# Kernel tuning notes

Hardware: AMD Instinct MI355X
Metric: run time of the kernel (lower is better)

Reference implementation:

```python
import jax, jax.numpy as jnp
import numpy as np

N = 50000      # nodes
E = 800000     # edges
F_IN = 128     # num_node_features
H = 128        # dim_h
C = 5          # num_classes
G = 8          # graphs in batch


def setup_inputs() -> dict:
    key = jax.random.key(0)
    ks = jax.random.split(key, 9)
    x = jax.random.normal(ks[0], (N, F_IN), dtype=jnp.float32)
    edge_index = jax.random.randint(ks[1], (2, E), 0, N, dtype=jnp.int64)
    batch = jnp.sort(jax.random.randint(ks[2], (N,), 0, G, dtype=jnp.int64))
    s1 = 1.0 / np.sqrt(F_IN)
    s2 = 1.0 / np.sqrt(H)
    sl = 1.0 / np.sqrt(2 * H)
    W1 = jax.random.uniform(ks[3], (F_IN, H), jnp.float32, -s1, s1)
    b1 = jnp.zeros((H,), jnp.float32)
    W2 = jax.random.uniform(ks[4], (H, H), jnp.float32, -s2, s2)
    b2 = jnp.zeros((H,), jnp.float32)
    Wl = jax.random.uniform(ks[5], (2 * H, C), jnp.float32, -sl, sl)
    bl = jax.random.uniform(ks[6], (C,), jnp.float32, -sl, sl)
    return {"x": x, "edge_index": edge_index, "batch": batch,
            "W1": W1, "b1": b1, "W2": W2, "b2": b2, "Wl": Wl, "bl": bl}


def gcn_conv(x, W, b, src, dst):
    # PyG GCNConv: X' = D^{-1/2} (A + I) D^{-1/2} X W + b
    xw = x @ W                                           # [N, H]
    # degree with self-loops: 1 + in-degree
    deg = jnp.ones((N,), xw.dtype).at[dst].add(1.0)      # [N]
    dinv = jax.lax.rsqrt(deg)                            # [N]
    norm = dinv[src] * dinv[dst]                         # [E]
    msg = xw[src] * norm[:, None]                        # [E, H] gather
    agg = jax.ops.segment_sum(msg, dst, num_segments=N)  # scatter-add
    agg = agg + xw * (dinv * dinv)[:, None]              # self-loop term
    return agg + b


def reference(x, edge_index, batch, W1, b1, W2, b2, Wl, bl):
    src, dst = edge_index[0], edge_index[1]
    # dropout p=0.6 is a no-op in eval mode
    h1 = jax.nn.relu(gcn_conv(x, W1, b1, src, dst))
    h2 = jax.nn.relu(gcn_conv(h1, W2, b2, src, dst))
    h = jnp.concatenate([h2, h1], axis=-1)               # [N, 2H]
    cnt = jax.ops.segment_sum(jnp.ones((N,), h.dtype), batch, num_segments=G)
    hG = jax.ops.segment_sum(h, batch, num_segments=G) / jnp.maximum(cnt, 1.0)[:, None]
    logits = hG @ Wl + bl                                # [G, C]
    return hG, jax.nn.log_softmax(logits, axis=1)
```

## Files before the change

### kernel.cpp

```cpp
#include <hip/hip_runtime.h>

#define N_NODES 50000
#define N_EDGES 800000
#define HDIM    128
#define NGRAPH  8
#define NCLS    5
#define SCAN_CHUNK 1024
#define NSCANBLK ((N_NODES + SCAN_CHUNK - 1) / SCAN_CHUNK)
#define NB_GEMM  ((N_NODES + 63) / 64)
#define NB_EDGE  ((N_EDGES + 255) / 256)

__device__ __forceinline__ float bf2f(ushort u) {
    return __uint_as_float((unsigned int)u << 16);
}
__device__ __forceinline__ ushort f2bf(float f) {
    unsigned int u = __float_as_uint(f);
    u += 0x7FFFu + ((u >> 16) & 1u);
    return (ushort)(u >> 16);
}

typedef __attribute__((ext_vector_type(8)))  __bf16 bf16x8;
typedef __attribute__((ext_vector_type(16))) float  f32x16;
typedef __attribute__((ext_vector_type(2)))  float  f32x2;
union BF8 { uint4 q; ushort u[8]; bf16x8 v; };

__global__ __launch_bounds__(256) void k_pre(const float* __restrict__ x,
                                             ushort* __restrict__ xb,
                                             const float* __restrict__ W1,
                                             const float* __restrict__ W2,
                                             ushort* __restrict__ Wt1,
                                             ushort* __restrict__ Wt2,
                                             int* cnti, float* hG) {
    int i = blockIdx.x * blockDim.x + threadIdx.x;
    if (i < N_NODES) cnti[i] = 0;
    if (i < NGRAPH * 2 * HDIM) hG[i] = 0.0f;
    if (i < HDIM * HDIM) {
        int k = i >> 7, c = i & (HDIM - 1);
        Wt1[c * HDIM + k] = f2bf(W1[i]);
        Wt2[c * HDIM + k] = f2bf(W2[i]);
    }
    if ((size_t)i * 8 < (size_t)N_NODES * HDIM) {
        float4 f0 = reinterpret_cast<const float4*>(x)[i * 2];
        float4 f1 = reinterpret_cast<const float4*>(x)[i * 2 + 1];
        uint4 o;
        o.x = (unsigned)f2bf(f0.x) | ((unsigned)f2bf(f0.y) << 16);
        o.y = (unsigned)f2bf(f0.z) | ((unsigned)f2bf(f0.w) << 16);
        o.z = (unsigned)f2bf(f1.x) | ((unsigned)f2bf(f1.y) << 16);
        o.w = (unsigned)f2bf(f1.z) | ((unsigned)f2bf(f1.w) << 16);
        reinterpret_cast<uint4*>(xb)[i] = o;
    }
}

__global__ __launch_bounds__(256) void k_count(const int* __restrict__ dst,
                                               int* cnti,
                                               ushort* __restrict__ slot16) {
    int e4 = blockIdx.x * blockDim.x + threadIdx.x;
    if (e4 < N_EDGES / 4) {
        int4 d = reinterpret_cast<const int4*>(dst)[e4];
        ushort4 s;
        s.x = (ushort)atomicAdd(&cnti[d.x], 1);
        s.y = (ushort)atomicAdd(&cnti[d.y], 1);
        s.z = (ushort)atomicAdd(&cnti[d.z], 1);
        s.w = (ushort)atomicAdd(&cnti[d.w], 1);
        reinterpret_cast<ushort4*>(slot16)[e4] = s;
    }
}

__global__ __launch_bounds__(256) void k_scan1(const int* __restrict__ cnti,
                                               int* __restrict__ rowptr,
                                               int* __restrict__ bsum,
                                               float* __restrict__ dinv) {
    __shared__ int wsum[4];
    int tid = threadIdx.x, lane = tid & 63, wid = tid >> 6;
    int i0 = blockIdx.x * SCAN_CHUNK + tid * 4;
    int v[4];
    int tsum = 0;
#pragma unroll
    for (int p = 0; p < 4; ++p) {
        int i = i0 + p;
        v[p] = (i < N_NODES) ? cnti[i] : 0;
        if (i < N_NODES) dinv[i] = rsqrtf(1.0f + (float)v[p]);
        tsum += v[p];
    }
    int sc = tsum;
#pragma unroll
    for (int off = 1; off < 64; off <<= 1) {
        int t = __shfl_up(sc, off, 64);
        if (lane >= off) sc += t;
    }
    if (lane == 63) wsum[wid] = sc;
    __syncthreads();
    int woff = 0;
    for (int w = 0; w < wid; ++w) woff += wsum[w];
    int excl = woff + sc - tsum;
#pragma unroll
    for (int p = 0; p < 4; ++p) {
        int i = i0 + p;
        if (i < N_NODES) rowptr[i] = excl;
        excl += v[p];
    }
    if (tid == 255) bsum[blockIdx.x] = woff + sc;
}

__global__ __launch_bounds__(256) void k_scan3(int* __restrict__ rowptr,
                                               const int* __restrict__ bsum) {
    __shared__ int soff;
    int tid = threadIdx.x;
    int chunk = blockIdx.x >> 2;
    if (tid < 64) {
        int v = (tid < chunk) ? bsum[tid] : 0;
#pragma unroll
        for (int off = 32; off; off >>= 1) v += __shfl_xor(v, off, 64);
        if (tid == 0) soff = v;
    }
    __syncthreads();
    int i = blockIdx.x * 256 + tid;
    if (i < N_NODES) rowptr[i] += soff;
    if (blockIdx.x == 0 && tid == 0) rowptr[N_NODES] = N_EDGES;
}

__global__ __launch_bounds__(256) void k_gemm_fill(const ushort* __restrict__ Xb,
                                                   const ushort* __restrict__ Wt,
                                                   unsigned char* __restrict__ Y,
                                                   const int* __restrict__ src,
                                                   const int* __restrict__ dst,
                                                   const int* __restrict__ rowptr,
                                                   const ushort* __restrict__ slot16,
                                                   ushort* __restrict__ csrc16) {
    if (blockIdx.x >= NB_GEMM) {
        int e = (blockIdx.x - NB_GEMM) * 256 + threadIdx.x;
        if (e < N_EDGES) {
            int d = dst[e];
            int pos = rowptr[d] + (int)slot16[e];
            csrc16[pos] = (ushort)src[e];
        }
        return;
    }
    int tid  = threadIdx.x;
    int lane = tid & 63;
    int wv   = tid >> 6;
    int c0   = wv * 32;
    int lrow = lane & 31;
    int kgrp = lane >> 5;

    bf16x8 bfrag[8];
    {
        const ushort* wp = Wt + (size_t)(c0 + lrow) * HDIM + kgrp * 8;
#pragma unroll
        for (int kc = 0; kc < 8; ++kc) {
            BF8 t;
            t.q = *reinterpret_cast<const uint4*>(wp + kc * 16);
            bfrag[kc] = t.v;
        }
    }
#pragma unroll
    for (int chunk = 0; chunk < 2; ++chunk) {
        int m0 = blockIdx.x * 64 + chunk * 32;
        if (m0 >= N_NODES) return;
        int arow = m0 + lrow;
        if (arow > N_NODES - 1) arow = N_NODES - 1;
        const ushort* xp = Xb + (size_t)arow * HDIM + kgrp * 8;
        f32x16 acc;
#pragma unroll
        for (int i = 0; i < 16; ++i) acc[i] = 0.f;
#pragma unroll
        for (int kc = 0; kc < 8; ++kc) {
            BF8 a;
            a.q = *reinterpret_cast<const uint4*>(xp + kc * 16);
            acc = __builtin_amdgcn_mfma_f32_32x32x16_bf16(a.v, bfrag[kc], acc, 0, 0, 0);
        }
#pragma unroll
        for (int r = 0; r < 16; r += 2) {
            unsigned pk = (unsigned)__builtin_amdgcn_cvt_pk_fp8_f32(acc[r], acc[r + 1], 0, false);
            int row0 = m0 + (r & 3) + 8 * (r >> 2) + 4 * kgrp;
            if (row0 < N_NODES)
                Y[(size_t)row0 * HDIM + c0 + lrow] = (unsigned char)(pk & 0xFF);
            if (row0 + 1 < N_NODES)
                Y[(size_t)(row0 + 1) * HDIM + c0 + lrow] = (unsigned char)((pk >> 8) & 0xFF);
        }
    }
}

__global__ __launch_bounds__(256) void k_gemm(const ushort* __restrict__ Xb,
                                              const ushort* __restrict__ Wt,
                                              unsigned char* __restrict__ Y) {
    int tid  = threadIdx.x;
    int lane = tid & 63;
    int wv   = tid >> 6;
    int c0   = wv * 32;
    int lrow = lane & 31;
    int kgrp = lane >> 5;

    bf16x8 bfrag[8];
    {
        const ushort* wp = Wt + (size_t)(c0 + lrow) * HDIM + kgrp * 8;
#pragma unroll
        for (int kc = 0; kc < 8; ++kc) {
            BF8 t;
            t.q = *reinterpret_cast<const uint4*>(wp + kc * 16);
            bfrag[kc] = t.v;
        }
    }
#pragma unroll
    for (int chunk = 0; chunk < 2; ++chunk) {
        int m0 = blockIdx.x * 64 + chunk * 32;
        if (m0 >= N_NODES) return;
        int arow = m0 + lrow;
        if (arow > N_NODES - 1) arow = N_NODES - 1;
        const ushort* xp = Xb + (size_t)arow * HDIM + kgrp * 8;
        f32x16 acc;
#pragma unroll
        for (int i = 0; i < 16; ++i) acc[i] = 0.f;
#pragma unroll
        for (int kc = 0; kc < 8; ++kc) {
            BF8 a;
            a.q = *reinterpret_cast<const uint4*>(xp + kc * 16);
            acc = __builtin_amdgcn_mfma_f32_32x32x16_bf16(a.v, bfrag[kc], acc, 0, 0, 0);
        }
#pragma unroll
        for (int r = 0; r < 16; r += 2) {
            unsigned pk = (unsigned)__builtin_amdgcn_cvt_pk_fp8_f32(acc[r], acc[r + 1], 0, false);
            int row0 = m0 + (r & 3) + 8 * (r >> 2) + 4 * kgrp;
            if (row0 < N_NODES)
                Y[(size_t)row0 * HDIM + c0 + lrow] = (unsigned char)(pk & 0xFF);
            if (row0 + 1 < N_NODES)
                Y[(size_t)(row0 + 1) * HDIM + c0 + lrow] = (unsigned char)((pk >> 8) & 0xFF);
        }
    }
}

__global__ __launch_bounds__(256) void k_agg(const unsigned char* __restrict__ y,
                                             const int* __restrict__ rowptr,
                                             const ushort* __restrict__ csrc16,
                                             const float* __restrict__ dinv,
                                             const float* __restrict__ bias,
                                             ushort* __restrict__ h) {
    int node = blockIdx.x * 4 + (threadIdx.x >> 6);
    if (node >= N_NODES) return;
    int lane = threadIdx.x & 63;
    int grp  = lane >> 5;
    int fl   = lane & 31;
    int e0 = rowptr[node], e1 = rowptr[node + 1];
    float di = dinv[node];
    float a0 = 0.f, a1 = 0.f, a2 = 0.f, a3 = 0.f;
    int j = e0;
    for (; j + 8 <= e1; j += 8) {
#pragma unroll
        for (int u = 0; u < 4; ++u) {
            int s = (int)csrc16[j + u * 2 + grp];
            float w = dinv[s];
            unsigned pk = *reinterpret_cast<const unsigned*>(y + (size_t)s * HDIM + fl * 4);
            f32x2 lo = __builtin_amdgcn_cvt_pk_f32_fp8(pk, false);
            f32x2 hi = __builtin_amdgcn_cvt_pk_f32_fp8(pk, true);
            a0 = fmaf(w, lo[0], a0);
            a1 = fmaf(w, lo[1], a1);
            a2 = fmaf(w, hi[0], a2);
            a3 = fmaf(w, hi[1], a3);
        }
    }
    for (; j < e1; j += 2) {
        int jj = j + grp;
        bool valid = jj < e1;
        int s = valid ? (int)csrc16[jj] : 0;
        float w = valid ? dinv[s] : 0.f;
        unsigned pk = *reinterpret_cast<const unsigned*>(y + (size_t)s * HDIM + fl * 4);
        f32x2 lo = __builtin_amdgcn_cvt_pk_f32_fp8(pk, false);
        f32x2 hi = __builtin_amdgcn_cvt_pk_f32_fp8(pk, true);
        a0 = fmaf(w, lo[0], a0);
        a1 = fmaf(w, lo[1], a1);
        a2 = fmaf(w, hi[0], a2);
        a3 = fmaf(w, hi[1], a3);
    }
    a0 += __shfl_xor(a0, 32, 64);
    a1 += __shfl_xor(a1, 32, 64);
    a2 += __shfl_xor(a2, 32, 64);
    a3 += __shfl_xor(a3, 32, 64);
    {
        unsigned pk = *reinterpret_cast<const unsigned*>(y + (size_t)node * HDIM + fl * 4);
        f32x2 lo = __builtin_amdgcn_cvt_pk_f32_fp8(pk, false);
        f32x2 hi = __builtin_amdgcn_cvt_pk_f32_fp8(pk, true);
        a0 = fmaf(di, lo[0], a0);
        a1 = fmaf(di, lo[1], a1);
        a2 = fmaf(di, hi[0], a2);
        a3 = fmaf(di, hi[1], a3);
    }
    float r0 = fmaxf(fmaf(a0, di, bias[fl * 4 + 0]), 0.f);
    float r1 = fmaxf(fmaf(a1, di, bias[fl * 4 + 1]), 0.f);
    float r2 = fmaxf(fmaf(a2, di, bias[fl * 4 + 2]), 0.f);
    float r3 = fmaxf(fmaf(a3, di, bias[fl * 4 + 3]), 0.f);
    if (grp == 0) {
        uint2 pk;
        pk.x = (unsigned)f2bf(r0) | ((unsigned)f2bf(r1) << 16);
        pk.y = (unsigned)f2bf(r2) | ((unsigned)f2bf(r3) << 16);
        *reinterpret_cast<uint2*>(h + (size_t)node * HDIM + fl * 4) = pk;
    }
}

__global__ __launch_bounds__(256) void k_pool(const ushort* __restrict__ h2,
                                              const ushort* __restrict__ h1,
                                              const int* __restrict__ batch,
                                              float* __restrict__ hG) {
    int f  = threadIdx.x;
    const ushort* srcp = (f < HDIM) ? h2 : h1;
    int ff = f & (HDIM - 1);
    int n0 = blockIdx.x * 64;
    int n1 = min(n0 + 64, N_NODES);
    int g = batch[n0];
    float run = 0.f;
    for (int n = n0; n < n1; ++n) {
        int gn = batch[n];
        if (gn != g) {
            atomicAdd(&hG[g * 256 + f], run);
            run = 0.f;
            g = gn;
        }
        run += bf2f(srcp[(size_t)n * HDIM + ff]);
    }
    atomicAdd(&hG[g * 256 + f], run);
}

__global__ __launch_bounds__(256) void k_final(const float* __restrict__ hG,
                                               const int* __restrict__ batch,
                                               const float* __restrict__ Wl,
                                               const float* __restrict__ bl,
                                               float* __restrict__ outp) {
    __shared__ float sH[NGRAPH * 2 * HDIM];
    __shared__ float sL[NGRAPH * NCLS];
    __shared__ int   sStart[NGRAPH + 1];
    int tid = threadIdx.x;
    if (tid <= NGRAPH) {
        int lo = 0, hi = N_NODES;
        while (lo < hi) {
            int mid = (lo + hi) >> 1;
            if (batch[mid] < tid) lo = mid + 1; else hi = mid;
        }
        sStart[tid] = lo;
    }
    __syncthreads();
    for (int i = tid; i < NGRAPH * 2 * HDIM; i += 256) {
        int g = i >> 8;
        float cnt = (float)(sStart[g + 1] - sStart[g]);
        float m = hG[i] / fmaxf(cnt, 1.0f);
        sH[i] = m;
        outp[i] = m;
    }
    __syncthreads();
    if (tid < NGRAPH * NCLS) {
        int g = tid / NCLS, c = tid % NCLS;
        float acc = bl[c];
        for (int k = 0; k < 2 * HDIM; ++k)
            acc += sH[g * 256 + k] * Wl[k * NCLS + c];
        sL[tid] = acc;
    }
    __syncthreads();
    if (tid < NGRAPH) {
        float mx = -1e30f;
        for (int c = 0; c < NCLS; ++c) mx = fmaxf(mx, sL[tid * NCLS + c]);
        float se = 0.f;
        for (int c = 0; c < NCLS; ++c) se += expf(sL[tid * NCLS + c] - mx);
        float lse = logf(se) + mx;
        for (int c = 0; c < NCLS; ++c)
            outp[NGRAPH * 2 * HDIM + tid * NCLS + c] = sL[tid * NCLS + c] - lse;
    }
}

extern "C" void kernel_launch(void* const* d_in, const int* in_sizes, int n_in,
                              void* d_out, int out_size, void* d_ws, size_t ws_size,
                              hipStream_t stream) {
    const float* x    = (const float*)d_in[0];
    const int*   eidx = (const int*)d_in[1];
    const int*   batch= (const int*)d_in[2];
    const float* W1   = (const float*)d_in[3];
    const float* b1   = (const float*)d_in[4];
    const float* W2   = (const float*)d_in[5];
    const float* b2   = (const float*)d_in[6];
    const float* Wl   = (const float*)d_in[7];
    const float* bl   = (const float*)d_in[8];
    float* outp = (float*)d_out;

    const int* src = eidx;
    const int* dst = eidx + N_EDGES;

    char* ws = (char*)d_ws;
    size_t off = 0;
    auto alloc = [&](size_t bytes) -> char* {
        char* p = ws + off;
        off += (bytes + 255) & ~(size_t)255;
        return p;
    };
    ushort*        xb    = (ushort*)alloc((size_t)N_NODES * HDIM * 2);
    unsigned char* y     = (unsigned char*)alloc((size_t)N_NODES * HDIM);
    ushort*        h1    = (ushort*)alloc((size_t)N_NODES * HDIM * 2);
    ushort*        h2    = (ushort*)alloc((size_t)N_NODES * HDIM * 2);
    ushort*        Wt1   = (ushort*)alloc((size_t)HDIM * HDIM * 2);
    ushort*        Wt2   = (ushort*)alloc((size_t)HDIM * HDIM * 2);
    float*         dinv  = (float*) alloc((size_t)N_NODES * 4);
    int*           cnti  = (int*)   alloc((size_t)N_NODES * 4);
    int*           rowptr= (int*)   alloc((size_t)(N_NODES + 1) * 4);
    int*           bsum  = (int*)   alloc((size_t)NSCANBLK * 4);
    ushort*        slot16= (ushort*)alloc((size_t)N_EDGES * 2);
    ushort*        csrc16= (ushort*)alloc((size_t)N_EDGES * 2);
    float*         hG    = (float*) alloc((size_t)NGRAPH * 2 * HDIM * 4);

    k_pre  <<<(N_NODES * HDIM / 8 + 255) / 256, 256, 0, stream>>>(x, xb, W1, W2, Wt1, Wt2, cnti, hG);
    k_count<<<(N_EDGES / 4 + 255) / 256, 256, 0, stream>>>(dst, cnti, slot16);
    k_scan1<<<NSCANBLK, 256, 0, stream>>>(cnti, rowptr, bsum, dinv);
    k_scan3<<<(N_NODES + 255) / 256, 256, 0, stream>>>(rowptr, bsum);

    k_gemm_fill<<<NB_GEMM + NB_EDGE, 256, 0, stream>>>(xb, Wt1, y,
                                                       src, dst, rowptr, slot16, csrc16);
    k_agg <<<(N_NODES + 3) / 4, 256, 0, stream>>>(y, rowptr, csrc16, dinv, b1, h1);
    k_gemm<<<NB_GEMM, 256, 0, stream>>>(h1, Wt2, y);
    k_agg <<<(N_NODES + 3) / 4, 256, 0, stream>>>(y, rowptr, csrc16, dinv, b2, h2);

    k_pool <<<(N_NODES + 63) / 64, 256, 0, stream>>>(h2, h1, batch, hG);
    k_final<<<1, 256, 0, stream>>>(hG, batch, Wl, bl, outp);

    (void)in_sizes; (void)n_in; (void)out_size; (void)ws_size;
}
```

Baseline: 187.1 us.

## Pad CSR rows to multiples of eight and prescale GEMM output by dinv

Each CSR row is padded to a multiple of 8 entries, with the padding pointing at a zero row appended to y. This lets the aggregation kernel load 8 source indices per uint4 and issue 8 independent gathers with no tail branches. The GEMM epilogues now multiply rows by dinv before the fp8 conversion, which removes the per-edge dinv[s] gather and its FMA weight in aggregation. The costs are extra padded gathers of the zero row, more csrc16 storage, and a serial padding loop in the scan kernel. Prescaling before fp8 quantization also slightly changes rounding.

Result: faster. 172.7 us (-7.7%).

```diff
diff --git a/kernel.cpp b/kernel.cpp
--- a/kernel.cpp
+++ b/kernel.cpp
@@ -5,6 +5,7 @@
 #define HDIM    128
 #define NGRAPH  8
 #define NCLS    5
+#define ZROW    50000
 #define SCAN_CHUNK 1024
 #define NSCANBLK ((N_NODES + SCAN_CHUNK - 1) / SCAN_CHUNK)
 #define NB_GEMM  ((N_NODES + 63) / 64)
@@ -30,10 +31,12 @@
                                              const float* __restrict__ W2,
                                              ushort* __restrict__ Wt1,
                                              ushort* __restrict__ Wt2,
-                                             int* cnti, float* hG) {
+                                             int* cnti, float* hG,
+                                             unsigned char* __restrict__ y) {
     int i = blockIdx.x * blockDim.x + threadIdx.x;
     if (i < N_NODES) cnti[i] = 0;
     if (i < NGRAPH * 2 * HDIM) hG[i] = 0.0f;
+    if (i < 32) reinterpret_cast<unsigned*>(y + (size_t)ZROW * HDIM)[i] = 0u;
     if (i < HDIM * HDIM) {
         int k = i >> 7, c = i & (HDIM - 1);
         Wt1[c * HDIM + k] = f2bf(W1[i]);
@@ -78,8 +81,9 @@
 #pragma unroll
     for (int p = 0; p < 4; ++p) {
         int i = i0 + p;
-        v[p] = (i < N_NODES) ? cnti[i] : 0;
-        if (i < N_NODES) dinv[i] = rsqrtf(1.0f + (float)v[p]);
+        int c = (i < N_NODES) ? cnti[i] : 0;
+        if (i < N_NODES) dinv[i] = rsqrtf(1.0f + (float)c);
+        v[p] = (c + 7) & ~7;
         tsum += v[p];
     }
     int sc = tsum;
@@ -103,7 +107,9 @@
 }
 
 __global__ __launch_bounds__(256) void k_scan3(int* __restrict__ rowptr,
-                                               const int* __restrict__ bsum) {
+                                               const int* __restrict__ bsum,
+                                               const int* __restrict__ cnti,
+                                               ushort* __restrict__ csrc16) {
     __shared__ int soff;
     int tid = threadIdx.x;
     int chunk = blockIdx.x >> 2;
@@ -115,12 +121,19 @@
     }
     __syncthreads();
     int i = blockIdx.x * 256 + tid;
-    if (i < N_NODES) rowptr[i] += soff;
-    if (blockIdx.x == 0 && tid == 0) rowptr[N_NODES] = N_EDGES;
+    if (i < N_NODES) {
+        int rp = rowptr[i] + soff;
+        rowptr[i] = rp;
+        int c  = cnti[i];
+        int ce = (c + 7) & ~7;
+        for (int p = c; p < ce; ++p) csrc16[rp + p] = (ushort)ZROW;
+        if (i == N_NODES - 1) rowptr[N_NODES] = rp + ce;
+    }
 }
 
 __global__ __launch_bounds__(256) void k_gemm_fill(const ushort* __restrict__ Xb,
                                                    const ushort* __restrict__ Wt,
+                                                   const float* __restrict__ dinv,
                                                    unsigned char* __restrict__ Y,
                                                    const int* __restrict__ src,
                                                    const int* __restrict__ dst,
@@ -171,8 +184,10 @@
         }
 #pragma unroll
         for (int r = 0; r < 16; r += 2) {
-            unsigned pk = (unsigned)__builtin_amdgcn_cvt_pk_fp8_f32(acc[r], acc[r + 1], 0, false);
             int row0 = m0 + (r & 3) + 8 * (r >> 2) + 4 * kgrp;
+            float d0 = (row0     < N_NODES) ? dinv[row0]     : 0.f;
+            float d1 = (row0 + 1 < N_NODES) ? dinv[row0 + 1] : 0.f;
+            unsigned pk = (unsigned)__builtin_amdgcn_cvt_pk_fp8_f32(acc[r] * d0, acc[r + 1] * d1, 0, false);
             if (row0 < N_NODES)
                 Y[(size_t)row0 * HDIM + c0 + lrow] = (unsigned char)(pk & 0xFF);
             if (row0 + 1 < N_NODES)
@@ -183,6 +198,7 @@
 
 __global__ __launch_bounds__(256) void k_gemm(const ushort* __restrict__ Xb,
                                               const ushort* __restrict__ Wt,
+                                              const float* __restrict__ dinv,
                                               unsigned char* __restrict__ Y) {
     int tid  = threadIdx.x;
     int lane = tid & 63;
@@ -219,8 +235,10 @@
         }
 #pragma unroll
         for (int r = 0; r < 16; r += 2) {
-            unsigned pk = (unsigned)__builtin_amdgcn_cvt_pk_fp8_f32(acc[r], acc[r + 1], 0, false);
             int row0 = m0 + (r & 3) + 8 * (r >> 2) + 4 * kgrp;
+            float d0 = (row0     < N_NODES) ? dinv[row0]     : 0.f;
+            float d1 = (row0 + 1 < N_NODES) ? dinv[row0 + 1] : 0.f;
+            unsigned pk = (unsigned)__builtin_amdgcn_cvt_pk_fp8_f32(acc[r] * d0, acc[r + 1] * d1, 0, false);
             if (row0 < N_NODES)
                 Y[(size_t)row0 * HDIM + c0 + lrow] = (unsigned char)(pk & 0xFF);
             if (row0 + 1 < N_NODES)
@@ -244,32 +262,39 @@
     float di = dinv[node];
     float a0 = 0.f, a1 = 0.f, a2 = 0.f, a3 = 0.f;
     int j = e0;
-    for (; j + 8 <= e1; j += 8) {
-#pragma unroll
-        for (int u = 0; u < 4; ++u) {
-            int s = (int)csrc16[j + u * 2 + grp];
-            float w = dinv[s];
-            unsigned pk = *reinterpret_cast<const unsigned*>(y + (size_t)s * HDIM + fl * 4);
-            f32x2 lo = __builtin_amdgcn_cvt_pk_f32_fp8(pk, false);
-            f32x2 hi = __builtin_amdgcn_cvt_pk_f32_fp8(pk, true);
-            a0 = fmaf(w, lo[0], a0);
-            a1 = fmaf(w, lo[1], a1);
-            a2 = fmaf(w, hi[0], a2);
-            a3 = fmaf(w, hi[1], a3);
-        }
-    }
-    for (; j < e1; j += 2) {
-        int jj = j + grp;
-        bool valid = jj < e1;
-        int s = valid ? (int)csrc16[jj] : 0;
-        float w = valid ? dinv[s] : 0.f;
-        unsigned pk = *reinterpret_cast<const unsigned*>(y + (size_t)s * HDIM + fl * 4);
-        f32x2 lo = __builtin_amdgcn_cvt_pk_f32_fp8(pk, false);
-        f32x2 hi = __builtin_amdgcn_cvt_pk_f32_fp8(pk, true);
-        a0 = fmaf(w, lo[0], a0);
-        a1 = fmaf(w, lo[1], a1);
-        a2 = fmaf(w, hi[0], a2);
-        a3 = fmaf(w, hi[1], a3);
+    for (; j + 16 <= e1; j += 16) {
+        uint4 iv = *reinterpret_cast<const uint4*>(csrc16 + j + grp * 8);
+        int s[8];
+        s[0] = iv.x & 0xFFFF; s[1] = iv.x >> 16;
+        s[2] = iv.y & 0xFFFF; s[3] = iv.y >> 16;
+        s[4] = iv.z & 0xFFFF; s[5] = iv.z >> 16;
+        s[6] = iv.w & 0xFFFF; s[7] = iv.w >> 16;
+        unsigned pkv[8];
+#pragma unroll
+        for (int k = 0; k < 8; ++k)
+            pkv[k] = *reinterpret_cast<const unsigned*>(y + (size_t)s[k] * HDIM + fl * 4);
+#pragma unroll
+        for (int k = 0; k < 8; ++k) {
+            f32x2 lo = __builtin_amdgcn_cvt_pk_f32_fp8(pkv[k], false);
+            f32x2 hi = __builtin_amdgcn_cvt_pk_f32_fp8(pkv[k], true);
+            a0 += lo[0]; a1 += lo[1]; a2 += hi[0]; a3 += hi[1];
+        }
+    }
+    if (j < e1) {
+        uint2 iv = *reinterpret_cast<const uint2*>(csrc16 + j + grp * 4);
+        int s[4];
+        s[0] = iv.x & 0xFFFF; s[1] = iv.x >> 16;
+        s[2] = iv.y & 0xFFFF; s[3] = iv.y >> 16;
+        unsigned pkv[4];
+#pragma unroll
+        for (int k = 0; k < 4; ++k)
+            pkv[k] = *reinterpret_cast<const unsigned*>(y + (size_t)s[k] * HDIM + fl * 4);
+#pragma unroll
+        for (int k = 0; k < 4; ++k) {
+            f32x2 lo = __builtin_amdgcn_cvt_pk_f32_fp8(pkv[k], false);
+            f32x2 hi = __builtin_amdgcn_cvt_pk_f32_fp8(pkv[k], true);
+            a0 += lo[0]; a1 += lo[1]; a2 += hi[0]; a3 += hi[1];
+        }
     }
     a0 += __shfl_xor(a0, 32, 64);
     a1 += __shfl_xor(a1, 32, 64);
@@ -279,10 +304,7 @@
         unsigned pk = *reinterpret_cast<const unsigned*>(y + (size_t)node * HDIM + fl * 4);
         f32x2 lo = __builtin_amdgcn_cvt_pk_f32_fp8(pk, false);
         f32x2 hi = __builtin_amdgcn_cvt_pk_f32_fp8(pk, true);
-        a0 = fmaf(di, lo[0], a0);
-        a1 = fmaf(di, lo[1], a1);
-        a2 = fmaf(di, hi[0], a2);
-        a3 = fmaf(di, hi[1], a3);
+        a0 += lo[0]; a1 += lo[1]; a2 += hi[0]; a3 += hi[1];
     }
     float r0 = fmaxf(fmaf(a0, di, bias[fl * 4 + 0]), 0.f);
     float r1 = fmaxf(fmaf(a1, di, bias[fl * 4 + 1]), 0.f);
@@ -389,7 +411,7 @@
         return p;
     };
     ushort*        xb    = (ushort*)alloc((size_t)N_NODES * HDIM * 2);
-    unsigned char* y     = (unsigned char*)alloc((size_t)N_NODES * HDIM);
+    unsigned char* y     = (unsigned char*)alloc((size_t)(N_NODES + 1) * HDIM);
     ushort*        h1    = (ushort*)alloc((size_t)N_NODES * HDIM * 2);
     ushort*        h2    = (ushort*)alloc((size_t)N_NODES * HDIM * 2);
     ushort*        Wt1   = (ushort*)alloc((size_t)HDIM * HDIM * 2);
@@ -399,18 +421,18 @@
     int*           rowptr= (int*)   alloc((size_t)(N_NODES + 1) * 4);
     int*           bsum  = (int*)   alloc((size_t)NSCANBLK * 4);
     ushort*        slot16= (ushort*)alloc((size_t)N_EDGES * 2);
-    ushort*        csrc16= (ushort*)alloc((size_t)N_EDGES * 2);
+    ushort*        csrc16= (ushort*)alloc((size_t)(N_EDGES + 8 * N_NODES) * 2);
     float*         hG    = (float*) alloc((size_t)NGRAPH * 2 * HDIM * 4);
 
-    k_pre  <<<(N_NODES * HDIM / 8 + 255) / 256, 256, 0, stream>>>(x, xb, W1, W2, Wt1, Wt2, cnti, hG);
+    k_pre  <<<(N_NODES * HDIM / 8 + 255) / 256, 256, 0, stream>>>(x, xb, W1, W2, Wt1, Wt2, cnti, hG, y);
     k_count<<<(N_EDGES / 4 + 255) / 256, 256, 0, stream>>>(dst, cnti, slot16);
     k_scan1<<<NSCANBLK, 256, 0, stream>>>(cnti, rowptr, bsum, dinv);
-    k_scan3<<<(N_NODES + 255) / 256, 256, 0, stream>>>(rowptr, bsum);
-
-    k_gemm_fill<<<NB_GEMM + NB_EDGE, 256, 0, stream>>>(xb, Wt1, y,
+    k_scan3<<<(N_NODES + 255) / 256, 256, 0, stream>>>(rowptr, bsum, cnti, csrc16);
+
+    k_gemm_fill<<<NB_GEMM + NB_EDGE, 256, 0, stream>>>(xb, Wt1, dinv, y,
                                                        src, dst, rowptr, slot16, csrc16);
     k_agg <<<(N_NODES + 3) / 4, 256, 0, stream>>>(y, rowptr, csrc16, dinv, b1, h1);
-    k_gemm<<<NB_GEMM, 256, 0, stream>>>(h1, Wt2, y);
+    k_gemm<<<NB_GEMM, 256, 0, stream>>>(h1, Wt2, dinv, y);
     k_agg <<<(N_NODES + 3) / 4, 256, 0, stream>>>(y, rowptr, csrc16, dinv, b2, h2);
 
     k_pool <<<(N_NODES + 63) / 64, 256, 0, stream>>>(h2, h1, batch, hG);
```
